# Performance work log

Measured on AMD Instinct MI355X. Metric: run time of the kernel, lower is better.

Reference implementation:

```python
import jax, jax.numpy as jnp
import numpy as np

N_NODES = 50000
N_EDGES = 800000
N_GRAPHS = 512
IN_DIM = 50
H = 128  # hidden_channels


def _init_linear(key, out_dim, in_dim, bias=True):
    k1, k2 = jax.random.split(key)
    bound = 1.0 / np.sqrt(in_dim)
    W = jax.random.uniform(k1, (out_dim, in_dim), jnp.float32, -bound, bound)
    if bias:
        b = jax.random.uniform(k2, (out_dim,), jnp.float32, -bound, bound)
        return W, b
    return W


def setup_inputs() -> dict:
    key = jax.random.key(0)
    ks = jax.random.split(key, 16)
    x = jax.random.normal(ks[0], (N_NODES, IN_DIM), jnp.float32)
    edge_index = jax.random.randint(ks[1], (2, N_EDGES), 0, N_NODES, jnp.int64)
    batch = jnp.sort(jax.random.randint(ks[2], (N_NODES,), 0, N_GRAPHS, jnp.int64))
    Wl1, bl1 = _init_linear(ks[3], H, IN_DIM)
    Wr1 = _init_linear(ks[4], H, IN_DIM, bias=False)
    Wl2, bl2 = _init_linear(ks[5], 2 * H, H)
    Wr2 = _init_linear(ks[6], 2 * H, H, bias=False)
    Wl3, bl3 = _init_linear(ks[7], 4 * H, 2 * H)
    Wr3 = _init_linear(ks[8], 4 * H, 2 * H, bias=False)
    Wf1, bf1 = _init_linear(ks[9], 2 * H, 4 * H)
    Wf2, bf2 = _init_linear(ks[10], H, 2 * H)
    Wo, bo = _init_linear(ks[11], 1, H)
    return dict(x=x, edge_index=edge_index, batch=batch,
                Wl1=Wl1, bl1=bl1, Wr1=Wr1,
                Wl2=Wl2, bl2=bl2, Wr2=Wr2,
                Wl3=Wl3, bl3=bl3, Wr3=Wr3,
                Wf1=Wf1, bf1=bf1, Wf2=Wf2, bf2=bf2, Wo=Wo, bo=bo)


def sage_conv(x, src, dst, deg_inv, Wl, bl, Wr):
    # mean-aggregate neighbor features at destination nodes, then linear
    agg = jax.ops.segment_sum(x[src], dst, num_segments=N_NODES) * deg_inv
    return agg @ Wl.T + bl + x @ Wr.T


def reference(x, edge_index, batch, Wl1, bl1, Wr1, Wl2, bl2, Wr2,
              Wl3, bl3, Wr3, Wf1, bf1, Wf2, bf2, Wo, bo):
    src, dst = edge_index[0], edge_index[1]
    deg = jax.ops.segment_sum(jnp.ones((N_EDGES,), x.dtype), dst, num_segments=N_NODES)
    deg_inv = (1.0 / jnp.maximum(deg, 1.0))[:, None]

    x1 = jax.nn.leaky_relu(sage_conv(x, src, dst, deg_inv, Wl1, bl1, Wr1))
    x2 = jax.nn.relu(sage_conv(x1, src, dst, deg_inv, Wl2, bl2, Wr2))
    x3 = jax.nn.relu(sage_conv(x2, src, dst, deg_inv, Wl3, bl3, Wr3))

    # global mean pool per graph
    pool_sum = jax.ops.segment_sum(x3, batch, num_segments=N_GRAPHS)
    cnt = jax.ops.segment_sum(jnp.ones((N_NODES,), x.dtype), batch, num_segments=N_GRAPHS)
    x_pool = pool_sum / jnp.maximum(cnt, 1.0)[:, None]

    x4 = jax.nn.relu(x_pool @ Wf1.T + bf1)
    x5 = jax.nn.relu(x4 @ Wf2.T + bf2)
    return jax.nn.sigmoid(x5 @ Wo.T + bo)
```

## Files before the change

kernel.cpp:

```cpp
#include <hip/hip_runtime.h>
#include <math.h>

#define N_NODES 50000
#define N_EDGES 800000
#define N_GRAPHS 512
#define M_PAD 50048
#define SEG_SZ 6250

typedef unsigned char u8;
typedef unsigned short u16;
typedef unsigned int u32;
typedef long i64;
using floatx4 = __attribute__((ext_vector_type(4))) float;
using floatx2 = __attribute__((ext_vector_type(2))) float;

__device__ __forceinline__ u8 f2fp8(float v) {
    return (u8)(__builtin_amdgcn_cvt_pk_fp8_f32(v, v, 0, false) & 0xFF);
}
__device__ __forceinline__ u32 pack4fp8(float a, float b, float c, float d) {
    u32 p = __builtin_amdgcn_cvt_pk_fp8_f32(a, b, 0, false);
    return __builtin_amdgcn_cvt_pk_fp8_f32(c, d, p, true);
}
__device__ __forceinline__ void acc16fp8(float* acc, uint4 u) {
    const u32 w[4] = {u.x, u.y, u.z, u.w};
    #pragma unroll
    for (int j = 0; j < 4; ++j) {
        floatx2 lo = __builtin_amdgcn_cvt_pk_f32_fp8((int)w[j], false);
        floatx2 hi = __builtin_amdgcn_cvt_pk_f32_fp8((int)w[j], true);
        acc[j * 4 + 0] += lo[0]; acc[j * 4 + 1] += lo[1];
        acc[j * 4 + 2] += hi[0]; acc[j * 4 + 3] += hi[1];
    }
}

__device__ __forceinline__ void load_lds16(const u8* g, u8* l) {
    __builtin_amdgcn_global_load_lds(
        (const __attribute__((address_space(1))) u32*)g,
        (__attribute__((address_space(3))) u32*)l, 16, 0, 0);
}
template<int N> __device__ __forceinline__ void waitcnt_vm() {
    __builtin_amdgcn_s_waitcnt(0x0F70 | N);
}
__device__ __forceinline__ void raw_barrier() {
    asm volatile("s_barrier" ::: "memory");
}

#define EPT 8
__global__ __launch_bounds__(256) void count_seg_kernel(const int* __restrict__ dst,
                                                        int* __restrict__ degi) {
    const int seg = blockIdx.x & 7;
    const int lo = seg * SEG_SZ, hi = lo + SEG_SZ;
    int e = (blockIdx.x >> 3) * (256 * EPT) + threadIdx.x;
    #pragma unroll
    for (int j = 0; j < EPT; ++j, e += 256) {
        if (e < N_EDGES) {
            int d = dst[e];
            if (d >= lo && d < hi) atomicAdd(&degi[d], 1);
        }
    }
}

__global__ __launch_bounds__(256) void fill_seg_kernel(const int* __restrict__ src,
                                                       const int* __restrict__ dst,
                                                       const int* __restrict__ starts,
                                                       int* __restrict__ cursor,
                                                       u16* __restrict__ csr) {
    const int seg = blockIdx.x & 7;
    const int lo = seg * SEG_SZ, hi = lo + SEG_SZ;
    int e = (blockIdx.x >> 3) * (256 * EPT) + threadIdx.x;
    #pragma unroll
    for (int j = 0; j < EPT; ++j, e += 256) {
        if (e < N_EDGES) {
            int d = dst[e];
            if (d >= lo && d < hi) {
                int p = atomicAdd(&cursor[d], 1);
                csr[starts[d] + p] = (u16)src[e];
            }
        }
    }
}

__global__ void scan1_kernel(const int* __restrict__ degi, int* __restrict__ starts,
                             int* __restrict__ bsum) {
    __shared__ int s[256];
    int t = threadIdx.x, i = blockIdx.x * 256 + t;
    int v = (i < N_NODES) ? degi[i] : 0;
    s[t] = v; __syncthreads();
    for (int off = 1; off < 256; off <<= 1) {
        int x = (t >= off) ? s[t - off] : 0;
        __syncthreads();
        s[t] += x;
        __syncthreads();
    }
    if (i < N_NODES) starts[i] = s[t] - v;
    if (t == 255) bsum[blockIdx.x] = s[255];
}

__global__ void scan2_kernel(const int* __restrict__ bsum, int* __restrict__ boff,
                             int* __restrict__ starts, int nb) {
    __shared__ int s[256];
    int t = threadIdx.x;
    int v = (t < nb) ? bsum[t] : 0;
    s[t] = v; __syncthreads();
    for (int off = 1; off < 256; off <<= 1) {
        int x = (t >= off) ? s[t - off] : 0;
        __syncthreads();
        s[t] += x;
        __syncthreads();
    }
    if (t < nb) boff[t] = s[t] - v;
    if (t == nb - 1) starts[N_NODES] = s[t];
}

__global__ void scan3_gstart_kernel(int* __restrict__ starts, const int* __restrict__ boff,
                                    const int* __restrict__ batch, int* __restrict__ gstart) {
    int i = blockIdx.x * 256 + threadIdx.x;
    if (i >= N_NODES) return;
    starts[i] += boff[blockIdx.x];
    int b = batch[i];
    int bp = (i == 0) ? -1 : batch[i - 1];
    for (int g = bp + 1; g <= b; ++g) gstart[g] = i;
    if (i == N_NODES - 1)
        for (int g = b + 1; g <= N_GRAPHS; ++g) gstart[g] = N_NODES;
}

__global__ void conv_all_kernel(const float* __restrict__ x,
                                const float* __restrict__ Wl1, const float* __restrict__ Wr1,
                                const float* __restrict__ Wl2, const float* __restrict__ Wr2,
                                const float* __restrict__ Wl3, const float* __restrict__ Wr3,
                                const float* __restrict__ Wf1, const float* __restrict__ Wf2,
                                u8* __restrict__ abuf1,
                                u8* __restrict__ wb1, u8* __restrict__ wb2,
                                u8* __restrict__ wb3,
                                float* __restrict__ Wf1T, float* __restrict__ Wf2T) {
    int i = blockIdx.x * blockDim.x + threadIdx.x;
    if (i < N_NODES * 16) {
        int n = i >> 4, c = (i & 15) * 4;
        float v[4];
        #pragma unroll
        for (int j = 0; j < 4; ++j) {
            int cc = c + j;
            v[j] = (cc < 50) ? x[n * 50 + cc] : 0.0f;
        }
        *(u32*)(abuf1 + (size_t)n * 128 + 64 + c) = pack4fp8(v[0], v[1], v[2], v[3]);
        return;
    }
    i -= N_NODES * 16;
    if (i < 128 * 64) {
        int o = i / 64, c = i % 64;
        float vl = (c < 50) ? Wl1[o * 50 + c] : 0.0f;
        float vr = (c < 50) ? Wr1[o * 50 + c] : 0.0f;
        wb1[(size_t)o * 128 + c] = f2fp8(vl);
        wb1[(size_t)o * 128 + 64 + c] = f2fp8(vr);
        return;
    }
    i -= 128 * 64;
    if (i < 256 * 128) {
        int o = i / 128, c = i % 128;
        wb2[(size_t)o * 256 + c] = f2fp8(Wl2[o * 128 + c]);
        wb2[(size_t)o * 256 + 128 + c] = f2fp8(Wr2[o * 128 + c]);
        return;
    }
    i -= 256 * 128;
    if (i < 512 * 256) {
        int o = i / 256, c = i % 256;
        wb3[(size_t)o * 512 + c] = f2fp8(Wl3[o * 256 + c]);
        wb3[(size_t)o * 512 + 256 + c] = f2fp8(Wr3[o * 256 + c]);
        return;
    }
    i -= 512 * 256;
    if (i < 256 * 512) {
        int o = i >> 9, k = i & 511;
        Wf1T[(size_t)k * 256 + o] = Wf1[(size_t)o * 512 + k];
        return;
    }
    i -= 256 * 512;
    if (i < 128 * 256) {
        int o = i >> 8, k = i & 255;
        Wf2T[(size_t)k * 128 + o] = Wf2[(size_t)o * 256 + k];
    }
}

template<int DINP>
__global__ __launch_bounds__(256) void csr_agg_kernel(const int* __restrict__ starts,
                                                      const u16* __restrict__ csr,
                                                      u8* __restrict__ abuf) {
    constexpr int STRIDE = 2 * DINP;
    constexpr int LPR = DINP / 16;
    constexpr int EPW = 64 / LPR;
    const int wave = threadIdx.x >> 6, lane = threadIdx.x & 63;
    const int n = blockIdx.x * 4 + wave;
    if (n >= N_NODES) return;
    const int sub = lane / LPR;
    const int li = lane % LPR;
    const int s0 = starts[n], s1 = starts[n + 1];

    float acc[16] = {};
    const u8* xin = abuf + DINP;

    int e = s0 + sub;
    for (; e + EPW < s1; e += 2 * EPW) {
        int i0 = csr[e], i1 = csr[e + EPW];
        uint4 u0 = *(const uint4*)(xin + (size_t)i0 * STRIDE + li * 16);
        uint4 u1 = *(const uint4*)(xin + (size_t)i1 * STRIDE + li * 16);
        acc16fp8(acc, u0);
        acc16fp8(acc, u1);
    }
    for (; e < s1; e += EPW) {
        int i0 = csr[e];
        uint4 u0 = *(const uint4*)(xin + (size_t)i0 * STRIDE + li * 16);
        acc16fp8(acc, u0);
    }

    #pragma unroll
    for (int off = 32; off >= LPR; off >>= 1) {
        #pragma unroll
        for (int c = 0; c < 16; ++c) acc[c] += __shfl_down(acc[c], off);
    }

    if (lane < LPR) {
        float sc = 1.0f / fmaxf((float)(s1 - s0), 1.0f);
        uint4 o;
        o.x = pack4fp8(acc[0] * sc, acc[1] * sc, acc[2] * sc, acc[3] * sc);
        o.y = pack4fp8(acc[4] * sc, acc[5] * sc, acc[6] * sc, acc[7] * sc);
        o.z = pack4fp8(acc[8] * sc, acc[9] * sc, acc[10] * sc, acc[11] * sc);
        o.w = pack4fp8(acc[12] * sc, acc[13] * sc, acc[14] * sc, acc[15] * sc);
        *(uint4*)(abuf + (size_t)n * STRIDE + li * 16) = o;
    }
}

template<int K, int NB, int ACT>
__global__ __launch_bounds__(256) void gemm_fp8_kernel(
    const u8* __restrict__ A, const u8* __restrict__ W,
    const float* __restrict__ bias,
    u8* __restrict__ out8, int gstride, int goff, int N)
{
    constexpr int NKB = K / 32;
    constexpr int MT = M_PAD / 128;
    constexpr int MCHUNK = (MT + 7) / 8;
    __shared__ __align__(16) u8 As[3][128 * 32];
    __shared__ __align__(16) u8 Bs[3][128 * 32];

    const int bx = blockIdx.x;
    const int xcd = bx & 7;
    const int seq = bx >> 3;
    const int n = seq % NB;
    const int m = xcd * MCHUNK + seq / NB;
    if (m >= MT) return;
    const int bm = m * 128;
    const int bn = n * 128;

    const int tid = threadIdx.x;
    const int wave = tid >> 6, lane = tid & 63;
    const int wm = (wave & 1) * 64, wn = (wave >> 1) * 64;
    const int lm = lane & 15, lq = lane >> 4;

    const int srow = wave * 32 + (lane >> 1);
    const int scol = ((lane & 1) ^ ((lane >> 3) & 1)) * 16;
    const u8* gA = A + (size_t)(bm + srow) * K + scol;
    const u8* gB = W + (size_t)(bn + srow) * K + scol;
    const int lbase = wave * 32 * 32;

    auto stage = [&](int s, int r) {
        const int ko = s * 32;
        load_lds16(gA + ko, &As[r][lbase]);
        load_lds16(gB + ko, &Bs[r][lbase]);
    };

    floatx4 acc[4][4] = {};

    stage(0, 0);
    stage(1, 1);

    const int csw = (((lq >> 1) ^ ((lm >> 2) & 1)) << 4) + (lq & 1) * 8;

    #pragma unroll
    for (int kb = 0; kb < NKB; ++kb) {
        if (kb + 2 < NKB) stage(kb + 2, (kb + 2) % 3);
        const int rem = NKB - 1 - kb;
        if (rem >= 2)      waitcnt_vm<4>();
        else if (rem == 1) waitcnt_vm<2>();
        else               waitcnt_vm<0>();
        raw_barrier();

        const int r = kb % 3;
        i64 af[4], bfr[4];
        #pragma unroll
        for (int mi = 0; mi < 4; ++mi)
            af[mi] = *(const i64*)&As[r][(wm + mi * 16 + lm) * 32 + csw];
        #pragma unroll
        for (int ni = 0; ni < 4; ++ni)
            bfr[ni] = *(const i64*)&Bs[r][(wn + ni * 16 + lm) * 32 + csw];
        #pragma unroll
        for (int mi = 0; mi < 4; ++mi)
            #pragma unroll
            for (int ni = 0; ni < 4; ++ni)
                acc[mi][ni] = __builtin_amdgcn_mfma_f32_16x16x32_fp8_fp8(
                    af[mi], bfr[ni], acc[mi][ni], 0, 0, 0);
        raw_barrier();
    }

    #pragma unroll
    for (int mi = 0; mi < 4; ++mi) {
        int node0 = bm + wm + mi * 16 + lq * 4;
        #pragma unroll
        for (int ni = 0; ni < 4; ++ni) {
            int o = bn + wn + ni * 16 + lm;
            float bi = bias[o];
            #pragma unroll
            for (int r = 0; r < 4; ++r) {
                int node = node0 + r;
                if (node >= N) continue;
                float v = acc[mi][ni][r] + bi;
                if (ACT == 0) v = (v > 0.0f) ? v : 0.01f * v;
                else          v = fmaxf(v, 0.0f);
                out8[(size_t)node * gstride + goff + o] = f2fp8(v);
            }
        }
    }
}

__global__ __launch_bounds__(256) void pool_kernel(
    const u8* __restrict__ x3, const int* __restrict__ gstart,
    float* __restrict__ pool)
{
    __shared__ float sacc[32][128];
    const int g = blockIdx.x >> 2;
    const int slab = blockIdx.x & 3;
    const int t = threadIdx.x;
    const int chain = t >> 3;
    const int li = t & 7;
    const int c0 = slab * 128 + li * 16;
    const int n0 = gstart[g], n1 = gstart[g + 1];

    float acc[16] = {};
    for (int n = n0 + chain; n < n1; n += 32) {
        uint4 u = *(const uint4*)(x3 + (size_t)n * 512 + c0);
        acc16fp8(acc, u);
    }
    #pragma unroll
    for (int j = 0; j < 16; ++j) sacc[chain][li * 16 + j] = acc[j];
    __syncthreads();
    if (t < 128) {
        float s = 0.0f;
        #pragma unroll
        for (int r = 0; r < 32; ++r) s += sacc[r][t];
        pool[(size_t)g * 512 + slab * 128 + t] = s;
    }
}

__global__ __launch_bounds__(256) void dense_head_kernel(
    const float* __restrict__ pool, const int* __restrict__ gstart,
    const float* __restrict__ Wf1T, const float* __restrict__ bf1,
    const float* __restrict__ Wf2T, const float* __restrict__ bf2,
    const float* __restrict__ Wo,  const float* __restrict__ bo,
    float* __restrict__ out)
{
    __shared__ float sp[512];
    __shared__ float s4[256];
    __shared__ float red[128];
    const int g = blockIdx.x;
    const int t = threadIdx.x;
    const float sc = 1.0f / fmaxf((float)(gstart[g + 1] - gstart[g]), 1.0f);

    sp[t]       = pool[(size_t)g * 512 + t] * sc;
    sp[t + 256] = pool[(size_t)g * 512 + 256 + t] * sc;
    __syncthreads();

    {
        float s = bf1[t];
        #pragma unroll 8
        for (int k = 0; k < 512; ++k) s += sp[k] * Wf1T[(size_t)k * 256 + t];
        s4[t] = fmaxf(s, 0.0f);
    }
    __syncthreads();
    if (t < 128) {
        float s = bf2[t];
        #pragma unroll 8
        for (int k = 0; k < 256; ++k) s += s4[k] * Wf2T[(size_t)k * 128 + t];
        red[t] = fmaxf(s, 0.0f) * Wo[t];
    }
    __syncthreads();
    for (int off = 64; off >= 1; off >>= 1) {
        if (t < off) red[t] += red[t + off];
        __syncthreads();
    }
    if (t == 0) out[g] = 1.0f / (1.0f + expf(-(red[0] + bo[0])));
}

extern "C" void kernel_launch(void* const* d_in, const int* in_sizes, int n_in,
                              void* d_out, int out_size, void* d_ws, size_t ws_size,
                              hipStream_t stream)
{
    const float* x     = (const float*)d_in[0];
    const int*   ei    = (const int*)  d_in[1];
    const int*   batch = (const int*)  d_in[2];
    const float* Wl1   = (const float*)d_in[3];
    const float* bl1   = (const float*)d_in[4];
    const float* Wr1   = (const float*)d_in[5];
    const float* Wl2   = (const float*)d_in[6];
    const float* bl2   = (const float*)d_in[7];
    const float* Wr2   = (const float*)d_in[8];
    const float* Wl3   = (const float*)d_in[9];
    const float* bl3   = (const float*)d_in[10];
    const float* Wr3   = (const float*)d_in[11];
    const float* Wf1   = (const float*)d_in[12];
    const float* bf1   = (const float*)d_in[13];
    const float* Wf2   = (const float*)d_in[14];
    const float* bf2   = (const float*)d_in[15];
    const float* Wo    = (const float*)d_in[16];
    const float* bo    = (const float*)d_in[17];

    const int* src = ei;
    const int* dst = ei + N_EDGES;

    char* p = (char*)d_ws;
    auto alloc = [&](size_t bytes) { char* r = p; p += (bytes + 255) & ~(size_t)255; return r; };
    int*   gstart = (int*)  alloc(513 * 4);
    float* pool   = (float*)alloc((size_t)512 * 512 * 4);
    float* Wf1T   = (float*)alloc((size_t)512 * 256 * 4);
    float* Wf2T   = (float*)alloc((size_t)256 * 128 * 4);
    u8*    abuf1  = (u8*)   alloc((size_t)M_PAD * 128);
    u8*    abuf2  = (u8*)   alloc((size_t)M_PAD * 256);
    u8*    abuf3  = (u8*)   alloc((size_t)M_PAD * 512);
    u8*    x3buf8 = (u8*)   alloc((size_t)M_PAD * 512);
    u8*    wb1    = (u8*)   alloc((size_t)128 * 128);
    u8*    wb2    = (u8*)   alloc((size_t)256 * 256);
    u8*    wb3    = (u8*)   alloc((size_t)512 * 512);
    char*  zbase  = p;
    int*   degi   = (int*)  alloc(50176 * 4);
    int*   cursor = (int*)  alloc(50176 * 4);
    size_t zbytes = (size_t)(p - zbase);
    int*   starts = (int*)  alloc(50432 * 4);
    int*   bsum   = (int*)  alloc(256 * 4);
    int*   boff   = (int*)  alloc(256 * 4);
    u16*   csr    = (u16*)  alloc((size_t)N_EDGES * 2);

    hipMemsetAsync(zbase, 0, zbytes, stream);
    const int SEG_BLOCKS = (N_EDGES + 256 * EPT - 1) / (256 * EPT);
    count_seg_kernel<<<SEG_BLOCKS * 8, 256, 0, stream>>>(dst, degi);
    scan1_kernel<<<196, 256, 0, stream>>>(degi, starts, bsum);
    scan2_kernel<<<1, 256, 0, stream>>>(bsum, boff, starts, 196);
    scan3_gstart_kernel<<<196, 256, 0, stream>>>(starts, boff, batch, gstart);
    fill_seg_kernel<<<SEG_BLOCKS * 8, 256, 0, stream>>>(src, dst, starts, cursor, csr);

    const int CONV_N = N_NODES * 16 + 128 * 64 + 256 * 128 + 512 * 256
                     + 256 * 512 + 128 * 256;
    conv_all_kernel<<<(CONV_N + 255) / 256, 256, 0, stream>>>(
        x, Wl1, Wr1, Wl2, Wr2, Wl3, Wr3, Wf1, Wf2,
        abuf1, wb1, wb2, wb3, Wf1T, Wf2T);

    const int GB = 12500;
    const int GEMM_GRID = 49 * 8;

    csr_agg_kernel<64><<<GB, 256, 0, stream>>>(starts, csr, abuf1);
    gemm_fp8_kernel<128, 1, 0><<<GEMM_GRID * 1, 256, 0, stream>>>(
        abuf1, wb1, bl1, abuf2, 256, 128, N_NODES);

    csr_agg_kernel<128><<<GB, 256, 0, stream>>>(starts, csr, abuf2);
    gemm_fp8_kernel<256, 2, 1><<<GEMM_GRID * 2, 256, 0, stream>>>(
        abuf2, wb2, bl2, abuf3, 512, 256, N_NODES);

    csr_agg_kernel<256><<<GB, 256, 0, stream>>>(starts, csr, abuf3);
    gemm_fp8_kernel<512, 4, 1><<<GEMM_GRID * 4, 256, 0, stream>>>(
        abuf3, wb3, bl3, x3buf8, 512, 0, N_NODES);

    pool_kernel<<<N_GRAPHS * 4, 256, 0, stream>>>(x3buf8, gstart, pool);
    dense_head_kernel<<<N_GRAPHS, 256, 0, stream>>>(
        pool, gstart, Wf1T, bf1, Wf2T, bf2, Wo, bo, (float*)d_out);
}
```

Before: 383.1 us.

## Fuse preprocessing launches, single-block scan, and double GEMM K-tile depth

The degree-count kernel and the fp8 conversion/transpose kernel are merged into one launch. The three-stage prefix scan plus gstart computation and cursor zeroing are folded into a single 1024-thread block. The memset now covers only degi. Separately, the fp8 GEMM stages 64-wide K tiles instead of 32, issuing two loads per operand with a new XOR swizzle and two MFMA half-steps per tile, which halves the barriers per K. The aim is to cut launch overhead and sync count, at the cost of a serial single-block scan and doubled LDS use per block, which may lower occupancy.

```diff
diff --git a/kernel.cpp b/kernel.cpp
--- a/kernel.cpp
+++ b/kernel.cpp
@@ -6,6 +6,9 @@
 #define N_GRAPHS 512
 #define M_PAD 50048
 #define SEG_SZ 6250
+#define EPT 8
+#define SEG_BLOCKS 391
+#define COUNT_BLOCKS (SEG_BLOCKS * 8)
 
 typedef unsigned char u8;
 typedef unsigned short u16;
@@ -44,19 +47,110 @@
     asm volatile("s_barrier" ::: "memory");
 }
 
-#define EPT 8
-__global__ __launch_bounds__(256) void count_seg_kernel(const int* __restrict__ dst,
-                                                        int* __restrict__ degi) {
-    const int seg = blockIdx.x & 7;
-    const int lo = seg * SEG_SZ, hi = lo + SEG_SZ;
-    int e = (blockIdx.x >> 3) * (256 * EPT) + threadIdx.x;
-    #pragma unroll
-    for (int j = 0; j < EPT; ++j, e += 256) {
-        if (e < N_EDGES) {
-            int d = dst[e];
-            if (d >= lo && d < hi) atomicAdd(&degi[d], 1);
+__global__ __launch_bounds__(256) void prep_kernel(
+    const int* __restrict__ dst, int* __restrict__ degi,
+    const float* __restrict__ x,
+    const float* __restrict__ Wl1, const float* __restrict__ Wr1,
+    const float* __restrict__ Wl2, const float* __restrict__ Wr2,
+    const float* __restrict__ Wl3, const float* __restrict__ Wr3,
+    const float* __restrict__ Wf1, const float* __restrict__ Wf2,
+    u8* __restrict__ abuf1,
+    u8* __restrict__ wb1, u8* __restrict__ wb2, u8* __restrict__ wb3,
+    float* __restrict__ Wf1T, float* __restrict__ Wf2T)
+{
+    if (blockIdx.x < COUNT_BLOCKS) {
+        const int bx = blockIdx.x;
+        const int seg = bx & 7;
+        const int lo = seg * SEG_SZ, hi = lo + SEG_SZ;
+        int e = (bx >> 3) * (256 * EPT) + threadIdx.x;
+        #pragma unroll
+        for (int j = 0; j < EPT; ++j, e += 256) {
+            if (e < N_EDGES) {
+                int d = dst[e];
+                if (d >= lo && d < hi) atomicAdd(&degi[d], 1);
+            }
         }
-    }
+        return;
+    }
+    int i = (blockIdx.x - COUNT_BLOCKS) * 256 + threadIdx.x;
+    if (i < N_NODES * 16) {
+        int n = i >> 4, c = (i & 15) * 4;
+        float v[4];
+        #pragma unroll
+        for (int j = 0; j < 4; ++j) {
+            int cc = c + j;
+            v[j] = (cc < 50) ? x[n * 50 + cc] : 0.0f;
+        }
+        *(u32*)(abuf1 + (size_t)n * 128 + 64 + c) = pack4fp8(v[0], v[1], v[2], v[3]);
+        return;
+    }
+    i -= N_NODES * 16;
+    if (i < 128 * 64) {
+        int o = i / 64, c = i % 64;
+        float vl = (c < 50) ? Wl1[o * 50 + c] : 0.0f;
+        float vr = (c < 50) ? Wr1[o * 50 + c] : 0.0f;
+        wb1[(size_t)o * 128 + c] = f2fp8(vl);
+        wb1[(size_t)o * 128 + 64 + c] = f2fp8(vr);
+        return;
+    }
+    i -= 128 * 64;
+    if (i < 256 * 128) {
+        int o = i / 128, c = i % 128;
+        wb2[(size_t)o * 256 + c] = f2fp8(Wl2[o * 128 + c]);
+        wb2[(size_t)o * 256 + 128 + c] = f2fp8(Wr2[o * 128 + c]);
+        return;
+    }
+    i -= 256 * 128;
+    if (i < 512 * 256) {
+        int o = i / 256, c = i % 256;
+        wb3[(size_t)o * 512 + c] = f2fp8(Wl3[o * 256 + c]);
+        wb3[(size_t)o * 512 + 256 + c] = f2fp8(Wr3[o * 256 + c]);
+        return;
+    }
+    i -= 512 * 256;
+    if (i < 256 * 512) {
+        int o = i >> 9, k = i & 511;
+        Wf1T[(size_t)k * 256 + o] = Wf1[(size_t)o * 512 + k];
+        return;
+    }
+    i -= 256 * 512;
+    if (i < 128 * 256) {
+        int o = i >> 8, k = i & 255;
+        Wf2T[(size_t)k * 128 + o] = Wf2[(size_t)o * 256 + k];
+    }
+}
+
+__global__ __launch_bounds__(1024) void scan_all_kernel(
+    const int* __restrict__ degi, int* __restrict__ starts,
+    const int* __restrict__ batch, int* __restrict__ gstart,
+    int* __restrict__ cursor)
+{
+    __shared__ int ps[1024];
+    const int t = threadIdx.x;
+    const int CH = 49;
+    const int lo = t * CH;
+    const int hi = (lo + CH < N_NODES) ? lo + CH : N_NODES;
+    int s = 0;
+    for (int i = lo; i < hi; ++i) s += degi[i];
+    ps[t] = s;
+    __syncthreads();
+    for (int off = 1; off < 1024; off <<= 1) {
+        int v = (t >= off) ? ps[t - off] : 0;
+        __syncthreads();
+        ps[t] += v;
+        __syncthreads();
+    }
+    int run = (t == 0) ? 0 : ps[t - 1];
+    for (int i = lo; i < hi; ++i) { starts[i] = run; run += degi[i]; }
+    if (t == 1023) starts[N_NODES] = ps[1023];
+    for (int i = lo; i < hi; ++i) {
+        int b = batch[i];
+        int bp = (i == 0) ? -1 : batch[i - 1];
+        for (int g = bp + 1; g <= b; ++g) gstart[g] = i;
+        if (i == N_NODES - 1)
+            for (int g = b + 1; g <= N_GRAPHS; ++g) gstart[g] = N_NODES;
+    }
+    for (int i = t; i < 50176; i += 1024) cursor[i] = 0;
 }
 
 __global__ __launch_bounds__(256) void fill_seg_kernel(const int* __restrict__ src,
@@ -76,107 +170,6 @@
                 csr[starts[d] + p] = (u16)src[e];
             }
         }
-    }
-}
-
-__global__ void scan1_kernel(const int* __restrict__ degi, int* __restrict__ starts,
-                             int* __restrict__ bsum) {
-    __shared__ int s[256];
-    int t = threadIdx.x, i = blockIdx.x * 256 + t;
-    int v = (i < N_NODES) ? degi[i] : 0;
-    s[t] = v; __syncthreads();
-    for (int off = 1; off < 256; off <<= 1) {
-        int x = (t >= off) ? s[t - off] : 0;
-        __syncthreads();
-        s[t] += x;
-        __syncthreads();
-    }
-    if (i < N_NODES) starts[i] = s[t] - v;
-    if (t == 255) bsum[blockIdx.x] = s[255];
-}
-
-__global__ void scan2_kernel(const int* __restrict__ bsum, int* __restrict__ boff,
-                             int* __restrict__ starts, int nb) {
-    __shared__ int s[256];
-    int t = threadIdx.x;
-    int v = (t < nb) ? bsum[t] : 0;
-    s[t] = v; __syncthreads();
-    for (int off = 1; off < 256; off <<= 1) {
-        int x = (t >= off) ? s[t - off] : 0;
-        __syncthreads();
-        s[t] += x;
-        __syncthreads();
-    }
-    if (t < nb) boff[t] = s[t] - v;
-    if (t == nb - 1) starts[N_NODES] = s[t];
-}
-
-__global__ void scan3_gstart_kernel(int* __restrict__ starts, const int* __restrict__ boff,
-                                    const int* __restrict__ batch, int* __restrict__ gstart) {
-    int i = blockIdx.x * 256 + threadIdx.x;
-    if (i >= N_NODES) return;
-    starts[i] += boff[blockIdx.x];
-    int b = batch[i];
-    int bp = (i == 0) ? -1 : batch[i - 1];
-    for (int g = bp + 1; g <= b; ++g) gstart[g] = i;
-    if (i == N_NODES - 1)
-        for (int g = b + 1; g <= N_GRAPHS; ++g) gstart[g] = N_NODES;
-}
-
-__global__ void conv_all_kernel(const float* __restrict__ x,
-                                const float* __restrict__ Wl1, const float* __restrict__ Wr1,
-                                const float* __restrict__ Wl2, const float* __restrict__ Wr2,
-                                const float* __restrict__ Wl3, const float* __restrict__ Wr3,
-                                const float* __restrict__ Wf1, const float* __restrict__ Wf2,
-                                u8* __restrict__ abuf1,
-                                u8* __restrict__ wb1, u8* __restrict__ wb2,
-                                u8* __restrict__ wb3,
-                                float* __restrict__ Wf1T, float* __restrict__ Wf2T) {
-    int i = blockIdx.x * blockDim.x + threadIdx.x;
-    if (i < N_NODES * 16) {
-        int n = i >> 4, c = (i & 15) * 4;
-        float v[4];
-        #pragma unroll
-        for (int j = 0; j < 4; ++j) {
-            int cc = c + j;
-            v[j] = (cc < 50) ? x[n * 50 + cc] : 0.0f;
-        }
-        *(u32*)(abuf1 + (size_t)n * 128 + 64 + c) = pack4fp8(v[0], v[1], v[2], v[3]);
-        return;
-    }
-    i -= N_NODES * 16;
-    if (i < 128 * 64) {
-        int o = i / 64, c = i % 64;
-        float vl = (c < 50) ? Wl1[o * 50 + c] : 0.0f;
-        float vr = (c < 50) ? Wr1[o * 50 + c] : 0.0f;
-        wb1[(size_t)o * 128 + c] = f2fp8(vl);
-        wb1[(size_t)o * 128 + 64 + c] = f2fp8(vr);
-        return;
-    }
-    i -= 128 * 64;
-    if (i < 256 * 128) {
-        int o = i / 128, c = i % 128;
-        wb2[(size_t)o * 256 + c] = f2fp8(Wl2[o * 128 + c]);
-        wb2[(size_t)o * 256 + 128 + c] = f2fp8(Wr2[o * 128 + c]);
-        return;
-    }
-    i -= 256 * 128;
-    if (i < 512 * 256) {
-        int o = i / 256, c = i % 256;
-        wb3[(size_t)o * 512 + c] = f2fp8(Wl3[o * 256 + c]);
-        wb3[(size_t)o * 512 + 256 + c] = f2fp8(Wr3[o * 256 + c]);
-        return;
-    }
-    i -= 512 * 256;
-    if (i < 256 * 512) {
-        int o = i >> 9, k = i & 511;
-        Wf1T[(size_t)k * 256 + o] = Wf1[(size_t)o * 512 + k];
-        return;
-    }
-    i -= 256 * 512;
-    if (i < 128 * 256) {
-        int o = i >> 8, k = i & 255;
-        Wf2T[(size_t)k * 128 + o] = Wf2[(size_t)o * 256 + k];
     }
 }
 
@@ -234,11 +227,11 @@
     const float* __restrict__ bias,
     u8* __restrict__ out8, int gstride, int goff, int N)
 {
-    constexpr int NKB = K / 32;
+    constexpr int NKB = K / 64;
     constexpr int MT = M_PAD / 128;
     constexpr int MCHUNK = (MT + 7) / 8;
-    __shared__ __align__(16) u8 As[3][128 * 32];
-    __shared__ __align__(16) u8 Bs[3][128 * 32];
+    __shared__ __align__(16) u8 As[3][128 * 64];
+    __shared__ __align__(16) u8 Bs[3][128 * 64];
 
     const int bx = blockIdx.x;
     const int xcd = bx & 7;
@@ -254,48 +247,52 @@
     const int wm = (wave & 1) * 64, wn = (wave >> 1) * 64;
     const int lm = lane & 15, lq = lane >> 4;
 
-    const int srow = wave * 32 + (lane >> 1);
-    const int scol = ((lane & 1) ^ ((lane >> 3) & 1)) * 16;
+    const int srow = wave * 32 + (lane >> 2);
+    const int scol = (((lane & 3) ^ ((lane >> 2) & 3)) << 4);
     const u8* gA = A + (size_t)(bm + srow) * K + scol;
     const u8* gB = W + (size_t)(bn + srow) * K + scol;
-    const int lbase = wave * 32 * 32;
+    const int lbase = wave * 32 * 64;
 
     auto stage = [&](int s, int r) {
-        const int ko = s * 32;
-        load_lds16(gA + ko, &As[r][lbase]);
-        load_lds16(gB + ko, &Bs[r][lbase]);
+        const int ko = s * 64;
+        load_lds16(gA + ko,                  &As[r][lbase]);
+        load_lds16(gA + (size_t)16 * K + ko, &As[r][lbase + 16 * 64]);
+        load_lds16(gB + ko,                  &Bs[r][lbase]);
+        load_lds16(gB + (size_t)16 * K + ko, &Bs[r][lbase + 16 * 64]);
     };
 
     floatx4 acc[4][4] = {};
 
     stage(0, 0);
-    stage(1, 1);
-
-    const int csw = (((lq >> 1) ^ ((lm >> 2) & 1)) << 4) + (lq & 1) * 8;
+    if (NKB > 1) stage(1, 1);
 
     #pragma unroll
     for (int kb = 0; kb < NKB; ++kb) {
         if (kb + 2 < NKB) stage(kb + 2, (kb + 2) % 3);
         const int rem = NKB - 1 - kb;
-        if (rem >= 2)      waitcnt_vm<4>();
-        else if (rem == 1) waitcnt_vm<2>();
+        if (rem >= 2)      waitcnt_vm<8>();
+        else if (rem == 1) waitcnt_vm<4>();
         else               waitcnt_vm<0>();
         raw_barrier();
 
         const int r = kb % 3;
-        i64 af[4], bfr[4];
-        #pragma unroll
-        for (int mi = 0; mi < 4; ++mi)
-            af[mi] = *(const i64*)&As[r][(wm + mi * 16 + lm) * 32 + csw];
-        #pragma unroll
-        for (int ni = 0; ni < 4; ++ni)
-            bfr[ni] = *(const i64*)&Bs[r][(wn + ni * 16 + lm) * 32 + csw];
-        #pragma unroll
-        for (int mi = 0; mi < 4; ++mi)
+        #pragma unroll
+        for (int h = 0; h < 2; ++h) {
+            i64 af[4], bfr[4];
+            const int cA = (((h * 2 + (lq >> 1)) ^ (lm & 3)) << 4) + (lq & 1) * 8;
+            #pragma unroll
+            for (int mi = 0; mi < 4; ++mi)
+                af[mi] = *(const i64*)&As[r][(wm + mi * 16 + lm) * 64 + cA];
             #pragma unroll
             for (int ni = 0; ni < 4; ++ni)
-                acc[mi][ni] = __builtin_amdgcn_mfma_f32_16x16x32_fp8_fp8(
-                    af[mi], bfr[ni], acc[mi][ni], 0, 0, 0);
+                bfr[ni] = *(const i64*)&Bs[r][(wn + ni * 16 + lm) * 64 + cA];
+            #pragma unroll
+            for (int mi = 0; mi < 4; ++mi)
+                #pragma unroll
+                for (int ni = 0; ni < 4; ++ni)
+                    acc[mi][ni] = __builtin_amdgcn_mfma_f32_16x16x32_fp8_fp8(
+                        af[mi], bfr[ni], acc[mi][ni], 0, 0, 0);
+        }
         raw_barrier();
     }
 
@@ -426,28 +423,20 @@
     u8*    wb1    = (u8*)   alloc((size_t)128 * 128);
     u8*    wb2    = (u8*)   alloc((size_t)256 * 256);
     u8*    wb3    = (u8*)   alloc((size_t)512 * 512);
-    char*  zbase  = p;
     int*   degi   = (int*)  alloc(50176 * 4);
     int*   cursor = (int*)  alloc(50176 * 4);
-    size_t zbytes = (size_t)(p - zbase);
     int*   starts = (int*)  alloc(50432 * 4);
-    int*   bsum   = (int*)  alloc(256 * 4);
-    int*   boff   = (int*)  alloc(256 * 4);
     u16*   csr    = (u16*)  alloc((size_t)N_EDGES * 2);
 
-    hipMemsetAsync(zbase, 0, zbytes, stream);
-    const int SEG_BLOCKS = (N_EDGES + 256 * EPT - 1) / (256 * EPT);
-    count_seg_kernel<<<SEG_BLOCKS * 8, 256, 0, stream>>>(dst, degi);
-    scan1_kernel<<<196, 256, 0, stream>>>(degi, starts, bsum);
-    scan2_kernel<<<1, 256, 0, stream>>>(bsum, boff, starts, 196);
-    scan3_gstart_kernel<<<196, 256, 0, stream>>>(starts, boff, batch, gstart);
-    fill_seg_kernel<<<SEG_BLOCKS * 8, 256, 0, stream>>>(src, dst, starts, cursor, csr);
-
+    hipMemsetAsync(degi, 0, 50176 * 4, stream);
     const int CONV_N = N_NODES * 16 + 128 * 64 + 256 * 128 + 512 * 256
                      + 256 * 512 + 128 * 256;
-    conv_all_kernel<<<(CONV_N + 255) / 256, 256, 0, stream>>>(
-        x, Wl1, Wr1, Wl2, Wr2, Wl3, Wr3, Wf1, Wf2,
+    const int CONV_BLOCKS = (CONV_N + 255) / 256;
+    prep_kernel<<<COUNT_BLOCKS + CONV_BLOCKS, 256, 0, stream>>>(
+        dst, degi, x, Wl1, Wr1, Wl2, Wr2, Wl3, Wr3, Wf1, Wf2,
         abuf1, wb1, wb2, wb3, Wf1T, Wf2T);
+    scan_all_kernel<<<1, 1024, 0, stream>>>(degi, starts, batch, gstart, cursor);
+    fill_seg_kernel<<<SEG_BLOCKS * 8, 256, 0, stream>>>(src, dst, starts, cursor, csr);
 
     const int GB = 12500;
     const int GEMM_GRID = 49 * 8;
```

New measurement: 522.6 us. +36.4%, slower.
